# Optimization experiments

Measured on AMD Instinct MI355X. Metric: run time of the kernel, lower is better.

The kernel has to match this reference:

```python
import jax, jax.numpy as jnp
import numpy as np

ALPHA = 0.2  # LeakyReLU negative slope
NEG = -1e10  # mask value, matches -10000000000.0


def _gat_head(feat, adj, W, a1, a2):
    # feat: [N, Fin], W: [Fin, Fout], a1/a2: [Fout]
    h = feat @ W                              # [N, Fout]
    s = h @ a1                                # [N] attn_for_self
    t = h @ a2                                # [N] attn_for_neighs
    logits = jax.nn.leaky_relu(s[:, None] + t[None, :], ALPHA)  # [N, N]
    logits = logits + NEG * (1.0 - adj)       # additive adjacency mask
    attn = jax.nn.softmax(logits, axis=-1)    # [N, N]
    return attn @ h                           # [N, Fout]


def setup_inputs() -> dict:
    key = jax.random.key(0)
    ks = jax.random.split(key, 9)
    N, NFEAT, NHID, NCLASS, H = 6144, 128, 64, 16, 4
    glorot = jax.nn.initializers.glorot_uniform()
    adj = (jax.random.uniform(ks[0], (N, N)) < 0.005).astype(jnp.float32)
    feature = jax.random.normal(ks[1], (N, NFEAT), dtype=jnp.float32)
    in0 = NFEAT * H
    W0 = jnp.stack([glorot(ks[2 + i], (in0, NHID), jnp.float32) for i in range(H)])  # [H,in0,NHID]
    a1_0 = jax.random.normal(ks[6], (H, NHID), dtype=jnp.float32) * 0.1
    a2_0 = jax.random.normal(ks[7], (H, NHID), dtype=jnp.float32) * 0.1
    Wout = glorot(ks[8], (NHID * H, NCLASS), jnp.float32)
    a1_out = jax.random.normal(jax.random.fold_in(key, 100), (NCLASS,), dtype=jnp.float32) * 0.1
    a2_out = jax.random.normal(jax.random.fold_in(key, 101), (NCLASS,), dtype=jnp.float32) * 0.1
    return {"adj": adj, "feature": feature, "W0": W0, "a1_0": a1_0, "a2_0": a2_0,
            "Wout": Wout, "a1_out": a1_out, "a2_out": a2_out}


def reference(adj, feature, W0, a1_0, a2_0, Wout, a1_out, a2_out):
    H = W0.shape[0]
    N = feature.shape[0]
    x = jnp.tile(feature, (1, H))  # [N, nfeat*H]
    # hidden layer: H heads, concat=True -> elu then concat along features
    heads = jax.vmap(_gat_head, in_axes=(None, None, 0, 0, 0))(x, adj, W0, a1_0, a2_0)  # [H,N,NHID]
    heads = jax.nn.elu(heads)
    x = jnp.transpose(heads, (1, 0, 2)).reshape(N, -1)  # [N, H*NHID]
    # output layer: concat=False (no elu inside), then elu + softmax in GAT.call
    out = _gat_head(x, adj, Wout, a1_out, a2_out)  # [N, nclass]
    out = jax.nn.elu(out)
    return jax.nn.softmax(out, axis=-1)
```

## Files before the change

### kernel.cpp

```cpp
#include <hip/hip_runtime.h>
#include <cstdint>
#include <math.h>

#define N 6144
#define FIN 128
#define FH 64
#define NHEADS 4
#define NC 16
#define CAP 512
#define ALPHA 0.2f
#define NT 16

__device__ __forceinline__ float wave_sum(float v) {
    #pragma unroll
    for (int off = 32; off >= 1; off >>= 1) v += __shfl_xor(v, off);
    return v;
}
__device__ __forceinline__ float wave_max(float v) {
    #pragma unroll
    for (int off = 32; off >= 1; off >>= 1) v = fmaxf(v, __shfl_xor(v, off));
    return v;
}

__global__ void k_reduce_w(const float* __restrict__ W0, float* __restrict__ weff) {
    int idx = blockIdx.x * 256 + threadIdx.x;
    if (idx >= NHEADS * FIN * FH) return;
    int f = idx & 63, k = (idx >> 6) & 127, h = idx >> 13;
    const float* base = W0 + (size_t)h * 512 * 64;
    float s = 0.f;
    #pragma unroll
    for (int r = 0; r < 4; r++) s += base[(size_t)(r * 128 + k) * 64 + f];
    weff[idx] = s;
}

__global__ void k_hgemm(const float* __restrict__ feat, const float* __restrict__ weff,
                        const float* __restrict__ a1, const float* __restrict__ a2,
                        float* __restrict__ hfeat, float* __restrict__ sb,
                        float* __restrict__ tb) {
    __shared__ float fl[NT * FIN];
    int tid = threadIdx.x;
    int n0 = blockIdx.x * NT;
    for (int idx = tid; idx < NT * FIN; idx += 256) fl[idx] = feat[(size_t)n0 * FIN + idx];
    __syncthreads();
    int f = tid & 63, h = tid >> 6;
    const float* wcol = weff + (size_t)h * FIN * FH + f;
    float acc[NT];
    #pragma unroll
    for (int nn = 0; nn < NT; nn++) acc[nn] = 0.f;
    for (int k = 0; k < FIN; k++) {
        float w = wcol[(size_t)k * FH];
        #pragma unroll
        for (int nn = 0; nn < NT; nn++) acc[nn] = fmaf(fl[nn * FIN + k], w, acc[nn]);
    }
    float a1v = a1[h * FH + f], a2v = a2[h * FH + f];
    #pragma unroll
    for (int nn = 0; nn < NT; nn++) {
        hfeat[((size_t)h * N + (n0 + nn)) * FH + f] = acc[nn];
        float s = wave_sum(acc[nn] * a1v);
        float t = wave_sum(acc[nn] * a2v);
        if ((tid & 63) == 0) {
            sb[h * N + n0 + nn] = s;
            tb[h * N + n0 + nn] = t;
        }
    }
}

__global__ void k_row(const float* __restrict__ adj, const float* __restrict__ hfeat,
                      const float* __restrict__ sb, const float* __restrict__ tb,
                      const float* __restrict__ wout, const float* __restrict__ a1o,
                      const float* __restrict__ a2o,
                      int* __restrict__ cols, int* __restrict__ deg,
                      float* __restrict__ h2, float* __restrict__ s2,
                      float* __restrict__ t2) {
    int i = blockIdx.x;
    int tid = threadIdx.x;
    int lane = tid & 63, h = tid >> 6;
    __shared__ int lidx[CAP];
    __shared__ float xrow[NHEADS * FH];
    __shared__ int cnt;
    if (tid == 0) cnt = 0;
    __syncthreads();

    const float4* rowv = (const float4*)(adj + (size_t)i * N);
    float4 rv[6];
    #pragma unroll
    for (int it = 0; it < 6; it++) rv[it] = rowv[it * 256 + tid];
    unsigned long long lmask = (1ull << lane) - 1ull;
    #pragma unroll
    for (int it = 0; it < 6; it++) {
        int jb = (it * 256 + tid) * 4;
        bool p[4] = {rv[it].x != 0.f, rv[it].y != 0.f, rv[it].z != 0.f, rv[it].w != 0.f};
        #pragma unroll
        for (int c = 0; c < 4; c++) {
            unsigned long long mm = __ballot(p[c]);
            int tot = __popcll(mm);
            if (tot) {
                int prefix = __popcll(mm & lmask);
                int wb;
                if (lane == 0) wb = atomicAdd(&cnt, tot);
                wb = __shfl(wb, 0);
                int pos = wb + prefix;
                if (p[c] && pos < CAP) lidx[pos] = jb + c;
            }
        }
    }
    __syncthreads();
    int d = cnt;
    if (tid == 0) deg[i] = d;
    for (int t = tid; t < min(d, CAP); t += 256) cols[(size_t)i * CAP + t] = lidx[t];

    int mode = (d == 0) ? 1 : (d > CAP ? 2 : 0);
    int count = (mode == 0) ? d : N;
    const float* trow = tb + (size_t)h * N;
    const float* hrow = hfeat + (size_t)h * N * FH;
    float si = sb[h * N + i];
    int q = lane >> 4, fo = (lane & 15) * 4;
    float m = -INFINITY, l = 0.f;
    float4 acc = {0.f, 0.f, 0.f, 0.f};
    for (int base = 0; base < count; base += 64) {
        int idx = base + lane;
        int j = 0; float lr = -INFINITY;
        if (idx < count) {
            j = (mode == 0) ? lidx[idx] : idx;
            bool ok = (mode != 2) || (adj[(size_t)i * N + j] != 0.f);
            if (ok) {
                float z = si + trow[j];
                lr = (z >= 0.f) ? z : ALPHA * z;
            }
        }
        float mc = wave_max(lr);
        float mn = fmaxf(m, mc);
        if (mn == -INFINITY) continue;
        float scale = (m == -INFINITY) ? 0.f : expf(m - mn);
        float w = (lr == -INFINITY) ? 0.f : expf(lr - mn);
        l = l * scale + wave_sum(w);
        acc.x *= scale; acc.y *= scale; acc.z *= scale; acc.w *= scale;
        int cn = min(64, count - base);
        #pragma unroll 4
        for (int b = 0; b < cn; b += 4) {
            float wb = __shfl(w, b + q);
            int jn = __shfl(j, b + q);
            float4 hv = *(const float4*)(hrow + (size_t)jn * FH + fo);
            acc.x = fmaf(wb, hv.x, acc.x);
            acc.y = fmaf(wb, hv.y, acc.y);
            acc.z = fmaf(wb, hv.z, acc.z);
            acc.w = fmaf(wb, hv.w, acc.w);
        }
        m = mn;
    }
    #pragma unroll
    for (int off = 16; off <= 32; off <<= 1) {
        acc.x += __shfl_xor(acc.x, off);
        acc.y += __shfl_xor(acc.y, off);
        acc.z += __shfl_xor(acc.z, off);
        acc.w += __shfl_xor(acc.w, off);
    }
    if (lane < 16) {
        float linv = 1.f / l;
        float4 o;
        o.x = acc.x * linv; o.y = acc.y * linv; o.z = acc.z * linv; o.w = acc.w * linv;
        o.x = (o.x > 0.f) ? o.x : expm1f(o.x);
        o.y = (o.y > 0.f) ? o.y : expm1f(o.y);
        o.z = (o.z > 0.f) ? o.z : expm1f(o.z);
        o.w = (o.w > 0.f) ? o.w : expm1f(o.w);
        *(float4*)(xrow + h * FH + fo) = o;
    }
    __syncthreads();

    if (h == 0) {
        int f = lane & 15, part = lane >> 4;
        float dot = 0.f;
        #pragma unroll
        for (int k = 0; k < 64; k++)
            dot = fmaf(xrow[part * 64 + k], wout[(size_t)(part * 64 + k) * NC + f], dot);
        dot += __shfl_xor(dot, 16);
        dot += __shfl_xor(dot, 32);
        if (lane < NC) h2[(size_t)i * NC + lane] = dot;
        float sv = (lane < NC) ? dot * a1o[lane] : 0.f;
        float tv = (lane < NC) ? dot * a2o[lane] : 0.f;
        sv = wave_sum(sv); tv = wave_sum(tv);
        if (lane == 0) { s2[i] = sv; t2[i] = tv; }
    }
}

__global__ void k_attn_out(const float* __restrict__ h2, const float* __restrict__ s2,
                           const float* __restrict__ t2, const int* __restrict__ cols,
                           const int* __restrict__ deg, const float* __restrict__ adj,
                           float* __restrict__ out) {
    int w = threadIdx.x >> 6, lane = threadIdx.x & 63;
    int i = blockIdx.x * 4 + w;
    int d = deg[i];
    int mode = (d == 0) ? 1 : (d > CAP ? 2 : 0);
    int count = (mode == 0) ? d : N;
    const int* crow = cols + (size_t)i * CAP;
    float si = s2[i];
    int f = lane & 15, q = lane >> 4;
    float m = -INFINITY, l = 0.f, acc = 0.f;
    for (int base = 0; base < count; base += 64) {
        int idx = base + lane;
        int j = 0; float lr = -INFINITY;
        if (idx < count) {
            j = (mode == 0) ? crow[idx] : idx;
            bool ok = (mode != 2) || (adj[(size_t)i * N + j] != 0.f);
            if (ok) {
                float z = si + t2[j];
                lr = (z >= 0.f) ? z : ALPHA * z;
            }
        }
        float mc = wave_max(lr);
        float mn = fmaxf(m, mc);
        if (mn == -INFINITY) continue;
        float scale = (m == -INFINITY) ? 0.f : expf(m - mn);
        float wv = (lr == -INFINITY) ? 0.f : expf(lr - mn);
        l = l * scale + wave_sum(wv);
        acc *= scale;
        int cn = min(64, count - base);
        #pragma unroll 4
        for (int b = 0; b < cn; b += 4) {
            float wb = __shfl(wv, b + q);
            int jn = __shfl(j, b + q);
            acc = fmaf(wb, h2[(size_t)jn * NC + f], acc);
        }
        m = mn;
    }
    acc += __shfl_xor(acc, 16);
    acc += __shfl_xor(acc, 32);
    float o = acc / l;
    o = (o > 0.f) ? o : expm1f(o);
    float mv = (lane < NC) ? o : -INFINITY;
    float mx = wave_max(mv);
    float e = (lane < NC) ? expf(o - mx) : 0.f;
    float se = wave_sum(e);
    if (lane < NC) out[(size_t)i * NC + lane] = e / se;
}

extern "C" void kernel_launch(void* const* d_in, const int* in_sizes, int n_in,
                              void* d_out, int out_size, void* d_ws, size_t ws_size,
                              hipStream_t stream) {
    const float* adj  = (const float*)d_in[0];
    const float* feat = (const float*)d_in[1];
    const float* W0   = (const float*)d_in[2];
    const float* a1_0 = (const float*)d_in[3];
    const float* a2_0 = (const float*)d_in[4];
    const float* Wout = (const float*)d_in[5];
    const float* a1o  = (const float*)d_in[6];
    const float* a2o  = (const float*)d_in[7];
    float* out = (float*)d_out;

    float* weff  = (float*)d_ws;
    float* hfeat = weff + 32768;
    float* sb    = hfeat + 1572864;
    float* tb    = sb + 24576;
    float* h2    = tb + 24576;
    float* s2    = h2 + 98304;
    float* t2    = s2 + 6144;
    int*   cols  = (int*)(t2 + 6144);
    int*   deg   = cols + (size_t)N * CAP;

    k_reduce_w<<<128, 256, 0, stream>>>(W0, weff);
    k_hgemm<<<N / NT, 256, 0, stream>>>(feat, weff, a1_0, a2_0, hfeat, sb, tb);
    k_row<<<N, 256, 0, stream>>>(adj, hfeat, sb, tb, Wout, a1o, a2o,
                                 cols, deg, h2, s2, t2);
    k_attn_out<<<N / 4, 256, 0, stream>>>(h2, s2, t2, cols, deg, adj, out);
}
```

Before: 262.2 us.

## Split hgemm per head with LDS-staged weights; compact adjacency via per-thread bitmask scan

The feature GEMM now launches one block per (row tile, head). Each block stages that head's 128x64 weight slice in shared memory and uses float4 feature reads, so each wave computes 4 rows with 64 output lanes. Separately, adjacency compaction in k_row replaces per-column ballots and shared-memory atomics with a per-thread 24-bit mask, a wave prefix scan and a block-level offset, followed by a scatter. This is meant to cut atomic and ballot overhead and raise GEMM parallelism, but it adds 32KB of LDS per hgemm block, which can lower occupancy, and the neighbor order in lidx changes.

```diff
diff --git a/kernel.cpp b/kernel.cpp
--- a/kernel.cpp
+++ b/kernel.cpp
@@ -38,29 +38,45 @@
                         float* __restrict__ hfeat, float* __restrict__ sb,
                         float* __restrict__ tb) {
     __shared__ float fl[NT * FIN];
+    __shared__ float wl[FIN * FH];
     int tid = threadIdx.x;
-    int n0 = blockIdx.x * NT;
+    int h = blockIdx.x & 3;
+    int n0 = (blockIdx.x >> 2) * NT;
     for (int idx = tid; idx < NT * FIN; idx += 256) fl[idx] = feat[(size_t)n0 * FIN + idx];
-    __syncthreads();
-    int f = tid & 63, h = tid >> 6;
-    const float* wcol = weff + (size_t)h * FIN * FH + f;
-    float acc[NT];
-    #pragma unroll
-    for (int nn = 0; nn < NT; nn++) acc[nn] = 0.f;
-    for (int k = 0; k < FIN; k++) {
-        float w = wcol[(size_t)k * FH];
+    {
+        const float4* wsrc = (const float4*)(weff + (size_t)h * FIN * FH);
+        float4* wdst = (float4*)wl;
+        for (int idx = tid; idx < FIN * FH / 4; idx += 256) wdst[idx] = wsrc[idx];
+    }
+    __syncthreads();
+    int lane = tid & 63, w = tid >> 6;
+    int r0 = w * 4;
+    float acc[4] = {0.f, 0.f, 0.f, 0.f};
+    #pragma unroll 2
+    for (int k = 0; k < FIN; k += 4) {
+        float w0 = wl[(k + 0) * FH + lane];
+        float w1 = wl[(k + 1) * FH + lane];
+        float w2 = wl[(k + 2) * FH + lane];
+        float w3 = wl[(k + 3) * FH + lane];
         #pragma unroll
-        for (int nn = 0; nn < NT; nn++) acc[nn] = fmaf(fl[nn * FIN + k], w, acc[nn]);
-    }
-    float a1v = a1[h * FH + f], a2v = a2[h * FH + f];
-    #pragma unroll
-    for (int nn = 0; nn < NT; nn++) {
-        hfeat[((size_t)h * N + (n0 + nn)) * FH + f] = acc[nn];
-        float s = wave_sum(acc[nn] * a1v);
-        float t = wave_sum(acc[nn] * a2v);
-        if ((tid & 63) == 0) {
-            sb[h * N + n0 + nn] = s;
-            tb[h * N + n0 + nn] = t;
+        for (int r = 0; r < 4; r++) {
+            float4 fv = *(const float4*)(&fl[(r0 + r) * FIN + k]);
+            acc[r] = fmaf(fv.x, w0, acc[r]);
+            acc[r] = fmaf(fv.y, w1, acc[r]);
+            acc[r] = fmaf(fv.z, w2, acc[r]);
+            acc[r] = fmaf(fv.w, w3, acc[r]);
+        }
+    }
+    float a1v = a1[h * FH + lane], a2v = a2[h * FH + lane];
+    #pragma unroll
+    for (int r = 0; r < 4; r++) {
+        int n = n0 + r0 + r;
+        hfeat[((size_t)h * N + n) * FH + lane] = acc[r];
+        float s = wave_sum(acc[r] * a1v);
+        float t = wave_sum(acc[r] * a2v);
+        if (lane == 0) {
+            sb[h * N + n] = s;
+            tb[h * N + n] = t;
         }
     }
 }
@@ -77,36 +93,44 @@
     int lane = tid & 63, h = tid >> 6;
     __shared__ int lidx[CAP];
     __shared__ float xrow[NHEADS * FH];
-    __shared__ int cnt;
-    if (tid == 0) cnt = 0;
-    __syncthreads();
+    __shared__ int wtot[4];
 
     const float4* rowv = (const float4*)(adj + (size_t)i * N);
     float4 rv[6];
     #pragma unroll
     for (int it = 0; it < 6; it++) rv[it] = rowv[it * 256 + tid];
-    unsigned long long lmask = (1ull << lane) - 1ull;
+
+    unsigned bm = 0;
     #pragma unroll
     for (int it = 0; it < 6; it++) {
-        int jb = (it * 256 + tid) * 4;
-        bool p[4] = {rv[it].x != 0.f, rv[it].y != 0.f, rv[it].z != 0.f, rv[it].w != 0.f};
-        #pragma unroll
-        for (int c = 0; c < 4; c++) {
-            unsigned long long mm = __ballot(p[c]);
-            int tot = __popcll(mm);
-            if (tot) {
-                int prefix = __popcll(mm & lmask);
-                int wb;
-                if (lane == 0) wb = atomicAdd(&cnt, tot);
-                wb = __shfl(wb, 0);
-                int pos = wb + prefix;
-                if (p[c] && pos < CAP) lidx[pos] = jb + c;
-            }
-        }
-    }
-    __syncthreads();
-    int d = cnt;
+        bm |= (rv[it].x != 0.f ? 1u : 0u) << (it * 4 + 0);
+        bm |= (rv[it].y != 0.f ? 1u : 0u) << (it * 4 + 1);
+        bm |= (rv[it].z != 0.f ? 1u : 0u) << (it * 4 + 2);
+        bm |= (rv[it].w != 0.f ? 1u : 0u) << (it * 4 + 3);
+    }
+    int cnt_t = __popc(bm);
+    int v = cnt_t;
+    #pragma unroll
+    for (int s = 1; s < 64; s <<= 1) {
+        int u = __shfl_up(v, s);
+        if (lane >= s) v += u;
+    }
+    if (lane == 63) wtot[h] = v;
+    __syncthreads();
+    int base = 0;
+    #pragma unroll
+    for (int wi = 0; wi < 4; wi++) base += (wi < h) ? wtot[wi] : 0;
+    int d = wtot[0] + wtot[1] + wtot[2] + wtot[3];
+    int off = base + v - cnt_t;
+    unsigned bits = bm;
+    while (bits) {
+        int b = __ffs(bits) - 1;
+        bits &= bits - 1;
+        int pos = off++;
+        if (pos < CAP) lidx[pos] = (b >> 2) * 1024 + tid * 4 + (b & 3);
+    }
     if (tid == 0) deg[i] = d;
+    __syncthreads();
     for (int t = tid; t < min(d, CAP); t += 256) cols[(size_t)i * CAP + t] = lidx[t];
 
     int mode = (d == 0) ? 1 : (d > CAP ? 2 : 0);
@@ -117,8 +141,8 @@
     int q = lane >> 4, fo = (lane & 15) * 4;
     float m = -INFINITY, l = 0.f;
     float4 acc = {0.f, 0.f, 0.f, 0.f};
-    for (int base = 0; base < count; base += 64) {
-        int idx = base + lane;
+    for (int bb = 0; bb < count; bb += 64) {
+        int idx = bb + lane;
         int j = 0; float lr = -INFINITY;
         if (idx < count) {
             j = (mode == 0) ? lidx[idx] : idx;
@@ -135,7 +159,7 @@
         float w = (lr == -INFINITY) ? 0.f : expf(lr - mn);
         l = l * scale + wave_sum(w);
         acc.x *= scale; acc.y *= scale; acc.z *= scale; acc.w *= scale;
-        int cn = min(64, count - base);
+        int cn = min(64, count - bb);
         #pragma unroll 4
         for (int b = 0; b < cn; b += 4) {
             float wb = __shfl(w, b + q);
@@ -149,11 +173,11 @@
         m = mn;
     }
     #pragma unroll
-    for (int off = 16; off <= 32; off <<= 1) {
-        acc.x += __shfl_xor(acc.x, off);
-        acc.y += __shfl_xor(acc.y, off);
-        acc.z += __shfl_xor(acc.z, off);
-        acc.w += __shfl_xor(acc.w, off);
+    for (int off2 = 16; off2 <= 32; off2 <<= 1) {
+        acc.x += __shfl_xor(acc.x, off2);
+        acc.y += __shfl_xor(acc.y, off2);
+        acc.z += __shfl_xor(acc.z, off2);
+        acc.w += __shfl_xor(acc.w, off2);
     }
     if (lane < 16) {
         float linv = 1.f / l;
@@ -196,8 +220,8 @@
     float si = s2[i];
     int f = lane & 15, q = lane >> 4;
     float m = -INFINITY, l = 0.f, acc = 0.f;
-    for (int base = 0; base < count; base += 64) {
-        int idx = base + lane;
+    for (int bb = 0; bb < count; bb += 64) {
+        int idx = bb + lane;
         int j = 0; float lr = -INFINITY;
         if (idx < count) {
             j = (mode == 0) ? crow[idx] : idx;
@@ -214,7 +238,7 @@
         float wv = (lr == -INFINITY) ? 0.f : expf(lr - mn);
         l = l * scale + wave_sum(wv);
         acc *= scale;
-        int cn = min(64, count - base);
+        int cn = min(64, count - bb);
         #pragma unroll 4
         for (int b = 0; b < cn; b += 4) {
             float wb = __shfl(wv, b + q);
@@ -258,7 +282,7 @@
     int*   deg   = cols + (size_t)N * CAP;
 
     k_reduce_w<<<128, 256, 0, stream>>>(W0, weff);
-    k_hgemm<<<N / NT, 256, 0, stream>>>(feat, weff, a1_0, a2_0, hfeat, sb, tb);
+    k_hgemm<<<(N / NT) * NHEADS, 256, 0, stream>>>(feat, weff, a1_0, a2_0, hfeat, sb, tb);
     k_row<<<N, 256, 0, stream>>>(adj, hfeat, sb, tb, Wout, a1o, a2o,
                                  cols, deg, h2, s2, t2);
     k_attn_out<<<N / 4, 256, 0, stream>>>(h2, s2, t2, cols, deg, adj, out);
```

New measurement: 262.2 us, median of 2. Within noise of the previous version (-0.0%).
